# Kernel tuning notes

Hardware: AMD Instinct MI355X
Metric: run time of the kernel (lower is better)

## Reference

```python
import jax, jax.numpy as jnp
import numpy as np

T = 1048576          # number of time steps in the trace
SIGMA_NUM = 8
EPSILON_NUM = 8
FEAT = 2 + SIGMA_NUM + EPSILON_NUM  # [t, r_obs, sigmas..., epsilons...]


def setup_inputs() -> dict:
    key = jax.random.key(0)
    ks = jax.random.split(key, 6)
    trace = jax.random.normal(ks[0], (T, FEAT), dtype=jnp.float32)
    # column 0 is time: sorted grid with small dt so the 1M-step recurrence stays bounded
    trace = trace.at[:, 0].set(jnp.arange(T, dtype=jnp.float32) * 1e-3)
    # column 1 row 0 is the initial rate; keep it positive-ish
    trace = trace.at[0, 1].set(0.05)
    sigma_W = jax.random.normal(ks[1], (1, SIGMA_NUM), dtype=jnp.float32) * 0.01
    sigma_b = jax.random.normal(ks[2], (1,), dtype=jnp.float32) * 0.01
    eps_W = jax.random.normal(ks[3], (1, EPSILON_NUM), dtype=jnp.float32) * 0.01
    k = jnp.abs(jax.random.normal(ks[4], (1,), dtype=jnp.float32)) * 0.1
    theta = jnp.abs(jax.random.normal(ks[5], (1,), dtype=jnp.float32)) * 0.05
    return {"trace_data": trace, "sigma_W": sigma_W, "sigma_b": sigma_b,
            "eps_W": eps_W, "k": k, "theta": theta}


def reference(trace_data, sigma_W, sigma_b, eps_W, k, theta):
    S, E = SIGMA_NUM, EPSILON_NUM
    t = trace_data[:, 0]
    dts = t[1:] - t[:-1]                                   # [T-1]
    # sigma/epsilon projections depend only on trace data -> vectorize outside scan
    sig = trace_data[:-1, 2:2 + S] @ sigma_W[0] + sigma_b[0]   # [T-1]
    eps = trace_data[:-1, 2 + S:2 + S + E] @ eps_W[0]          # [T-1]
    kk = k[0]
    th = theta[0]
    r0 = trace_data[0, 1]

    def step(r, x):
        dt, s, e = x
        ode = r + kk * (th - r) * dt
        sde = s * jnp.sqrt(jnp.abs(r * dt)) * e
        r_next = ode + sde
        return r_next, r_next

    _, r_predicts = jax.lax.scan(step, r0, (dts, sig, eps))   # [T-1]
    regs = 2.0 * kk * th - sig ** 2                           # [T-1]
    return r_predicts, regs, dts
```

## Files before the change

kernel.cpp:

```cpp
#include <hip/hip_runtime.h>
#include <math.h>

#define NSTEPS  1048575
#define NPAD    1048576
#define FEAT    18
#define CLEN    64
#define CHUNKS  (NPAD / CLEN)
#define SCANT   1024
#define PERT    (CHUNKS / SCANT)

__global__ void prep_kernel(const float* __restrict__ trace,
                            const float* __restrict__ sW, const float* __restrict__ sb,
                            const float* __restrict__ eW, const float* __restrict__ kp,
                            const float* __restrict__ thp,
                            float2* __restrict__ dc, float* __restrict__ out)
{
    int n = blockIdx.x * blockDim.x + threadIdx.x;
    if (n >= NSTEPS) { dc[n] = make_float2(0.f, 0.f); return; }
    const float* row = trace + (long)n * FEAT;
    float d = row[FEAT] - row[0];
    float sig = sb[0];
#pragma unroll
    for (int j = 0; j < 8; ++j) sig = fmaf(row[2 + j], sW[j], sig);
    float ep = 0.f;
#pragma unroll
    for (int j = 0; j < 8; ++j) ep = fmaf(row[10 + j], eW[j], ep);
    float k = kp[0], th = thp[0];
    dc[n] = make_float2(d, sig * ep * sqrtf(fabsf(d)));
    out[NSTEPS + n]     = fmaf(-sig, sig, 2.f * k * th);
    out[2 * NSTEPS + n] = d;
}

#define GSTEP(dd, cc) { \
    float a   = fmaf(-k, (dd), 1.f); \
    float b   = kth * (dd); \
    float ar  = fabsf(r); \
    float sq  = sqrtf(ar); \
    float inv = (ar > 1e-30f) ? rsqrtf(ar) : 0.f; \
    float g   = fmaf(0.5f * (cc), copysignf(inv, r), a); \
    r = fmaf((cc), sq, fmaf(a, r, b)); \
    P *= g; }

__global__ void chunk_pass(const float2* __restrict__ dc,
                           const float* __restrict__ trace,
                           const float* __restrict__ kp, const float* __restrict__ thp,
                           float2* __restrict__ ab)
{
    int c = blockIdx.x * blockDim.x + threadIdx.x;
    float k = kp[0], th = thp[0];
    float kth = k * th;
    float r0 = trace[1];
    float tc = trace[(long)c * CLEN * FEAT];
    float t0 = trace[0];
    float s = th + (r0 - th) * __expf(-k * (tc - t0));
    const float4* q = (const float4*)(dc + (long)c * CLEN);
    float4 buf[32];
#pragma unroll
    for (int i = 0; i < 32; ++i) buf[i] = q[i];
    float r = s, P = 1.f;
#pragma unroll
    for (int i = 0; i < 32; ++i) {
        GSTEP(buf[i].x, buf[i].y)
        GSTEP(buf[i].z, buf[i].w)
    }
    ab[c] = make_float2(P, fmaf(-P, s, r));
}

__device__ __forceinline__ void wave_scan_affine(float& A, float& B, int lane) {
#pragma unroll
    for (int d = 1; d < 64; d <<= 1) {
        float pA = __shfl_up(A, d, 64);
        float pB = __shfl_up(B, d, 64);
        if (lane >= d) { B = fmaf(A, pB, B); A *= pA; }
    }
}

__global__ void __launch_bounds__(SCANT) correct_scan(const float2* __restrict__ ab,
                                                      const float* __restrict__ trace,
                                                      float* __restrict__ s_new)
{
    __shared__ float wAs[16], wBs[16];
    int t = threadIdx.x, lane = t & 63, wid = t >> 6;
    const float4* q = (const float4*)(ab + t * PERT);
    float A[PERT], B[PERT];
#pragma unroll
    for (int i = 0; i < PERT / 2; ++i) {
        float4 v = q[i];
        A[2 * i] = v.x; B[2 * i] = v.y;
        A[2 * i + 1] = v.z; B[2 * i + 1] = v.w;
    }
    float aggA = 1.f, aggB = 0.f;
#pragma unroll
    for (int j = 0; j < PERT; ++j) { aggB = fmaf(A[j], aggB, B[j]); aggA *= A[j]; }
    float iA = aggA, iB = aggB;
    wave_scan_affine(iA, iB, lane);
    if (lane == 63) { wAs[wid] = iA; wBs[wid] = iB; }
    __syncthreads();
    if (wid == 0) {
        float aA = (lane < 16) ? wAs[lane] : 1.f;
        float aB = (lane < 16) ? wBs[lane] : 0.f;
        wave_scan_affine(aA, aB, lane);
        if (lane < 16) { wAs[lane] = aA; wBs[lane] = aB; }
    }
    __syncthreads();
    float weA = 1.f, weB = 0.f;
    if (wid > 0) { weA = wAs[wid - 1]; weB = wBs[wid - 1]; }
    float eA = __shfl_up(iA, 1, 64), eB = __shfl_up(iB, 1, 64);
    if (lane == 0) { eA = 1.f; eB = 0.f; }
    float xA = eA * weA;
    float xB = fmaf(eA, weB, eB);
    float r0 = trace[1];
    float x = fmaf(xA, r0, xB);
#pragma unroll
    for (int i = 0; i < PERT / 4; ++i) {
        float4 ov;
        ov.x = x; x = fmaf(A[4 * i + 0], x, B[4 * i + 0]);
        ov.y = x; x = fmaf(A[4 * i + 1], x, B[4 * i + 1]);
        ov.z = x; x = fmaf(A[4 * i + 2], x, B[4 * i + 2]);
        ov.w = x; x = fmaf(A[4 * i + 3], x, B[4 * i + 3]);
        ((float4*)(s_new + t * PERT))[i] = ov;
    }
}

#define FSTEP(dd, cc) { \
    float a = fmaf(-k, (dd), 1.f); \
    float b = kth * (dd); \
    r = fmaf((cc), sqrtf(fabsf(r)), fmaf(a, r, b)); }

__global__ void final_pass(const float2* __restrict__ dc,
                           const float* __restrict__ starts,
                           const float* __restrict__ kp, const float* __restrict__ thp,
                           float* __restrict__ out)
{
    int c = blockIdx.x * blockDim.x + threadIdx.x;
    float r = starts[c];
    float k = kp[0], th = thp[0];
    float kth = k * th;
    const float4* q = (const float4*)(dc + (long)c * CLEN);
    float4 buf[32];
#pragma unroll
    for (int i = 0; i < 32; ++i) buf[i] = q[i];
    int nb = c * CLEN;
#pragma unroll
    for (int i = 0; i < 16; ++i) {
        float4 ov;
        FSTEP(buf[2 * i].x, buf[2 * i].y)         ov.x = r;
        FSTEP(buf[2 * i].z, buf[2 * i].w)         ov.y = r;
        FSTEP(buf[2 * i + 1].x, buf[2 * i + 1].y) ov.z = r;
        FSTEP(buf[2 * i + 1].z, buf[2 * i + 1].w) ov.w = r;
        int n0 = nb + 4 * i;
        if (n0 + 4 <= NSTEPS) {
            *(float4*)(out + n0) = ov;
        } else {
            if (n0 + 0 < NSTEPS) out[n0 + 0] = ov.x;
            if (n0 + 1 < NSTEPS) out[n0 + 1] = ov.y;
            if (n0 + 2 < NSTEPS) out[n0 + 2] = ov.z;
        }
    }
}

extern "C" void kernel_launch(void* const* d_in, const int* in_sizes, int n_in,
                              void* d_out, int out_size, void* d_ws, size_t ws_size,
                              hipStream_t stream)
{
    const float* trace = (const float*)d_in[0];
    const float* sW    = (const float*)d_in[1];
    const float* sb    = (const float*)d_in[2];
    const float* eW    = (const float*)d_in[3];
    const float* kp    = (const float*)d_in[4];
    const float* thp   = (const float*)d_in[5];
    float* out = (float*)d_out;

    float*  w     = (float*)d_ws;
    float2* dc    = (float2*)w;
    float2* ab    = (float2*)(w + 2 * NPAD);
    float*  s_new = w + 2 * NPAD + 2 * CHUNKS;

    prep_kernel<<<NPAD / 256, 256, 0, stream>>>(trace, sW, sb, eW, kp, thp, dc, out);
    chunk_pass<<<CHUNKS / 256, 256, 0, stream>>>(dc, trace, kp, thp, ab);
    correct_scan<<<1, SCANT, 0, stream>>>(ab, trace, s_new);
    final_pass<<<CHUNKS / 256, 256, 0, stream>>>(dc, s_new, kp, thp, out);
}
```

Before: 142.6 us.

## Fuse chunk, scan and final passes into one grid-synchronized kernel

Replaces the three post-prep kernels (chunk linearization, single-block scan, final replay) with one fused kernel using 4-step chunks. Each 1024-thread block scans its chunks' affine maps, publishes a block aggregate, and spins on a global atomic counter until all 256 blocks arrive. Every block then redundantly scans the 256 aggregates in shared memory and replays its steps. Chunk seeds move into the prep kernel, which also loads rows as float2 pairs. This removes two launches and the serial single-block scan. In exchange it depends on all 256 blocks being co-resident to avoid deadlock, and short chunks mean less linearization error averaging.

```diff
diff --git a/kernel.cpp b/kernel.cpp
--- a/kernel.cpp
+++ b/kernel.cpp
@@ -4,31 +4,42 @@
 #define NSTEPS  1048575
 #define NPAD    1048576
 #define FEAT    18
-#define CLEN    64
+#define CLEN    4
 #define CHUNKS  (NPAD / CLEN)
-#define SCANT   1024
-#define PERT    (CHUNKS / SCANT)
+#define K2B     256
+#define K2T     1024
 
 __global__ void prep_kernel(const float* __restrict__ trace,
                             const float* __restrict__ sW, const float* __restrict__ sb,
                             const float* __restrict__ eW, const float* __restrict__ kp,
                             const float* __restrict__ thp,
-                            float2* __restrict__ dc, float* __restrict__ out)
+                            float2* __restrict__ dc, float* __restrict__ seeds,
+                            float* __restrict__ out, unsigned int* __restrict__ cnt)
 {
     int n = blockIdx.x * blockDim.x + threadIdx.x;
+    if (n == 0) *cnt = 0;
     if (n >= NSTEPS) { dc[n] = make_float2(0.f, 0.f); return; }
-    const float* row = trace + (long)n * FEAT;
-    float d = row[FEAT] - row[0];
+    const float2* r2 = (const float2*)(trace + (long)n * FEAT);
+    float2 e0 = r2[0], e1 = r2[1], e2 = r2[2], e3 = r2[3], e4 = r2[4];
+    float2 e5 = r2[5], e6 = r2[6], e7 = r2[7], e8 = r2[8];
+    float tn1 = trace[(long)(n + 1) * FEAT];
+    float d = tn1 - e0.x;
     float sig = sb[0];
-#pragma unroll
-    for (int j = 0; j < 8; ++j) sig = fmaf(row[2 + j], sW[j], sig);
+    sig = fmaf(e1.x, sW[0], sig); sig = fmaf(e1.y, sW[1], sig);
+    sig = fmaf(e2.x, sW[2], sig); sig = fmaf(e2.y, sW[3], sig);
+    sig = fmaf(e3.x, sW[4], sig); sig = fmaf(e3.y, sW[5], sig);
+    sig = fmaf(e4.x, sW[6], sig); sig = fmaf(e4.y, sW[7], sig);
     float ep = 0.f;
-#pragma unroll
-    for (int j = 0; j < 8; ++j) ep = fmaf(row[10 + j], eW[j], ep);
+    ep = fmaf(e5.x, eW[0], ep); ep = fmaf(e5.y, eW[1], ep);
+    ep = fmaf(e6.x, eW[2], ep); ep = fmaf(e6.y, eW[3], ep);
+    ep = fmaf(e7.x, eW[4], ep); ep = fmaf(e7.y, eW[5], ep);
+    ep = fmaf(e8.x, eW[6], ep); ep = fmaf(e8.y, eW[7], ep);
     float k = kp[0], th = thp[0];
     dc[n] = make_float2(d, sig * ep * sqrtf(fabsf(d)));
     out[NSTEPS + n]     = fmaf(-sig, sig, 2.f * k * th);
     out[2 * NSTEPS + n] = d;
+    if ((n & 3) == 0)
+        seeds[n >> 2] = th + (trace[1] - th) * __expf(-k * (e0.x - trace[0]));
 }
 
 #define GSTEP(dd, cc) { \
@@ -41,30 +52,10 @@
     r = fmaf((cc), sq, fmaf(a, r, b)); \
     P *= g; }
 
-__global__ void chunk_pass(const float2* __restrict__ dc,
-                           const float* __restrict__ trace,
-                           const float* __restrict__ kp, const float* __restrict__ thp,
-                           float2* __restrict__ ab)
-{
-    int c = blockIdx.x * blockDim.x + threadIdx.x;
-    float k = kp[0], th = thp[0];
-    float kth = k * th;
-    float r0 = trace[1];
-    float tc = trace[(long)c * CLEN * FEAT];
-    float t0 = trace[0];
-    float s = th + (r0 - th) * __expf(-k * (tc - t0));
-    const float4* q = (const float4*)(dc + (long)c * CLEN);
-    float4 buf[32];
-#pragma unroll
-    for (int i = 0; i < 32; ++i) buf[i] = q[i];
-    float r = s, P = 1.f;
-#pragma unroll
-    for (int i = 0; i < 32; ++i) {
-        GSTEP(buf[i].x, buf[i].y)
-        GSTEP(buf[i].z, buf[i].w)
-    }
-    ab[c] = make_float2(P, fmaf(-P, s, r));
-}
+#define FSTEP(dd, cc) { \
+    float a = fmaf(-k, (dd), 1.f); \
+    float b = kth * (dd); \
+    rr = fmaf((cc), sqrtf(fabsf(rr)), fmaf(a, rr, b)); }
 
 __device__ __forceinline__ void wave_scan_affine(float& A, float& B, int lane) {
 #pragma unroll
@@ -75,24 +66,31 @@
     }
 }
 
-__global__ void __launch_bounds__(SCANT) correct_scan(const float2* __restrict__ ab,
-                                                      const float* __restrict__ trace,
-                                                      float* __restrict__ s_new)
+__global__ void __launch_bounds__(K2T) fused_pass(
+    const float2* __restrict__ dc, const float* __restrict__ seeds,
+    const float* __restrict__ trace,
+    const float* __restrict__ kp, const float* __restrict__ thp,
+    float* __restrict__ out,
+    float* __restrict__ gA, float* __restrict__ gB,
+    unsigned int* __restrict__ cnt)
 {
     __shared__ float wAs[16], wBs[16];
-    int t = threadIdx.x, lane = t & 63, wid = t >> 6;
-    const float4* q = (const float4*)(ab + t * PERT);
-    float A[PERT], B[PERT];
-#pragma unroll
-    for (int i = 0; i < PERT / 2; ++i) {
-        float4 v = q[i];
-        A[2 * i] = v.x; B[2 * i] = v.y;
-        A[2 * i + 1] = v.z; B[2 * i + 1] = v.w;
-    }
-    float aggA = 1.f, aggB = 0.f;
-#pragma unroll
-    for (int j = 0; j < PERT; ++j) { aggB = fmaf(A[j], aggB, B[j]); aggA *= A[j]; }
-    float iA = aggA, iB = aggB;
+    __shared__ float sgA[K2B], sgB[K2B];
+    const int tid = threadIdx.x, lane = tid & 63, wid = tid >> 6, bid = blockIdx.x;
+    const int c = bid * K2T + tid;
+    const float k = kp[0], th = thp[0], kth = k * th;
+    const float4 q0 = ((const float4*)dc)[2 * c];
+    const float4 q1 = ((const float4*)dc)[2 * c + 1];
+    const float s = seeds[c];
+
+    float r = s, P = 1.f;
+    GSTEP(q0.x, q0.y)
+    GSTEP(q0.z, q0.w)
+    GSTEP(q1.x, q1.y)
+    GSTEP(q1.z, q1.w)
+    float A = P, B = fmaf(-P, s, r);
+
+    float iA = A, iB = B;
     wave_scan_affine(iA, iB, lane);
     if (lane == 63) { wAs[wid] = iA; wBs[wid] = iB; }
     __syncthreads();
@@ -107,55 +105,49 @@
     if (wid > 0) { weA = wAs[wid - 1]; weB = wBs[wid - 1]; }
     float eA = __shfl_up(iA, 1, 64), eB = __shfl_up(iB, 1, 64);
     if (lane == 0) { eA = 1.f; eB = 0.f; }
-    float xA = eA * weA;
-    float xB = fmaf(eA, weB, eB);
-    float r0 = trace[1];
-    float x = fmaf(xA, r0, xB);
-#pragma unroll
-    for (int i = 0; i < PERT / 4; ++i) {
-        float4 ov;
-        ov.x = x; x = fmaf(A[4 * i + 0], x, B[4 * i + 0]);
-        ov.y = x; x = fmaf(A[4 * i + 1], x, B[4 * i + 1]);
-        ov.z = x; x = fmaf(A[4 * i + 2], x, B[4 * i + 2]);
-        ov.w = x; x = fmaf(A[4 * i + 3], x, B[4 * i + 3]);
-        ((float4*)(s_new + t * PERT))[i] = ov;
+    float Ate = eA * weA;
+    float Bte = fmaf(eA, weB, eB);
+
+    if (tid == 0) {
+        __hip_atomic_store(&gA[bid], wAs[15], __ATOMIC_RELAXED, __HIP_MEMORY_SCOPE_AGENT);
+        __hip_atomic_store(&gB[bid], wBs[15], __ATOMIC_RELAXED, __HIP_MEMORY_SCOPE_AGENT);
+        __hip_atomic_fetch_add(cnt, 1u, __ATOMIC_ACQ_REL, __HIP_MEMORY_SCOPE_AGENT);
+        while (__hip_atomic_load(cnt, __ATOMIC_ACQUIRE, __HIP_MEMORY_SCOPE_AGENT) < K2B)
+            __builtin_amdgcn_s_sleep(1);
     }
-}
+    __syncthreads();
 
-#define FSTEP(dd, cc) { \
-    float a = fmaf(-k, (dd), 1.f); \
-    float b = kth * (dd); \
-    r = fmaf((cc), sqrtf(fabsf(r)), fmaf(a, r, b)); }
+    if (tid < K2B) {
+        sgA[tid] = __hip_atomic_load(&gA[tid], __ATOMIC_RELAXED, __HIP_MEMORY_SCOPE_AGENT);
+        sgB[tid] = __hip_atomic_load(&gB[tid], __ATOMIC_RELAXED, __HIP_MEMORY_SCOPE_AGENT);
+    }
+    __syncthreads();
+    for (int d = 1; d < K2B; d <<= 1) {
+        float pA = 1.f, pB = 0.f;
+        bool act = (tid < K2B) && (tid >= d);
+        if (act) { pA = sgA[tid - d]; pB = sgB[tid - d]; }
+        __syncthreads();
+        if (act) { sgB[tid] = fmaf(sgA[tid], pB, sgB[tid]); sgA[tid] *= pA; }
+        __syncthreads();
+    }
+    float beA = 1.f, beB = 0.f;
+    if (bid > 0) { beA = sgA[bid - 1]; beB = sgB[bid - 1]; }
 
-__global__ void final_pass(const float2* __restrict__ dc,
-                           const float* __restrict__ starts,
-                           const float* __restrict__ kp, const float* __restrict__ thp,
-                           float* __restrict__ out)
-{
-    int c = blockIdx.x * blockDim.x + threadIdx.x;
-    float r = starts[c];
-    float k = kp[0], th = thp[0];
-    float kth = k * th;
-    const float4* q = (const float4*)(dc + (long)c * CLEN);
-    float4 buf[32];
-#pragma unroll
-    for (int i = 0; i < 32; ++i) buf[i] = q[i];
-    int nb = c * CLEN;
-#pragma unroll
-    for (int i = 0; i < 16; ++i) {
-        float4 ov;
-        FSTEP(buf[2 * i].x, buf[2 * i].y)         ov.x = r;
-        FSTEP(buf[2 * i].z, buf[2 * i].w)         ov.y = r;
-        FSTEP(buf[2 * i + 1].x, buf[2 * i + 1].y) ov.z = r;
-        FSTEP(buf[2 * i + 1].z, buf[2 * i + 1].w) ov.w = r;
-        int n0 = nb + 4 * i;
-        if (n0 + 4 <= NSTEPS) {
-            *(float4*)(out + n0) = ov;
-        } else {
-            if (n0 + 0 < NSTEPS) out[n0 + 0] = ov.x;
-            if (n0 + 1 < NSTEPS) out[n0 + 1] = ov.y;
-            if (n0 + 2 < NSTEPS) out[n0 + 2] = ov.z;
-        }
+    float FA = Ate * beA;
+    float FB = fmaf(Ate, beB, Bte);
+    float rr = fmaf(FA, trace[1], FB);
+    float4 ov;
+    FSTEP(q0.x, q0.y) ov.x = rr;
+    FSTEP(q0.z, q0.w) ov.y = rr;
+    FSTEP(q1.x, q1.y) ov.z = rr;
+    FSTEP(q1.z, q1.w) ov.w = rr;
+    int nb = 4 * c;
+    if (nb + 4 <= NSTEPS) {
+        *(float4*)(out + nb) = ov;
+    } else {
+        out[nb + 0] = ov.x;
+        out[nb + 1] = ov.y;
+        out[nb + 2] = ov.z;
     }
 }
 
@@ -171,13 +163,14 @@
     const float* thp   = (const float*)d_in[5];
     float* out = (float*)d_out;
 
-    float*  w     = (float*)d_ws;
-    float2* dc    = (float2*)w;
-    float2* ab    = (float2*)(w + 2 * NPAD);
-    float*  s_new = w + 2 * NPAD + 2 * CHUNKS;
+    float*        w     = (float*)d_ws;
+    float2*       dc    = (float2*)w;
+    float*        seeds = w + 2 * NPAD;
+    float*        gA    = seeds + CHUNKS;
+    float*        gB    = gA + K2B;
+    unsigned int* cnt   = (unsigned int*)(gB + K2B);
 
-    prep_kernel<<<NPAD / 256, 256, 0, stream>>>(trace, sW, sb, eW, kp, thp, dc, out);
-    chunk_pass<<<CHUNKS / 256, 256, 0, stream>>>(dc, trace, kp, thp, ab);
-    correct_scan<<<1, SCANT, 0, stream>>>(ab, trace, s_new);
-    final_pass<<<CHUNKS / 256, 256, 0, stream>>>(dc, s_new, kp, thp, out);
+    prep_kernel<<<NPAD / 256, 256, 0, stream>>>(trace, sW, sb, eW, kp, thp,
+                                                dc, seeds, out, cnt);
+    fused_pass<<<K2B, K2T, 0, stream>>>(dc, seeds, trace, kp, thp, out, gA, gB, cnt);
 }
```

Result: faster. 128.7 us (-9.7%).
